# Performance work log

Hardware: AMD Instinct MI355X
Metric: run time of the kernel (lower is better)

Reference implementation:

```python
import jax, jax.numpy as jnp
import numpy as np

B, S, E, H = 2, 2048, 1024, 16
HD = E // H


def setup_inputs() -> dict:
    key = jax.random.key(0)
    ks = jax.random.split(key, 5)
    scale = 0.02
    return {
        "x": jax.random.normal(ks[0], (B, S, E), dtype=jnp.float32),
        "qkv_w": jax.random.normal(ks[1], (3 * E, E), dtype=jnp.float32) * scale,
        "qkv_b": jax.random.normal(ks[2], (3 * E,), dtype=jnp.float32) * scale,
        "out_w": jax.random.normal(ks[3], (E, E), dtype=jnp.float32) * scale,
        "out_b": jax.random.normal(ks[4], (E,), dtype=jnp.float32) * scale,
    }


def reference(x, qkv_w, qkv_b, out_w, out_b):
    b, s, e = x.shape
    scale = 1.0 / jnp.sqrt(jnp.float32(HD))
    # fused QKV projection: torch Linear is x @ W.T + b
    qkv = x @ qkv_w.T + qkv_b                       # [b, s, 3e]
    qkv = qkv.reshape(b, s, 3, H, HD)
    qkv = jnp.transpose(qkv, (2, 0, 3, 1, 4))       # [3, b, h, s, hd]
    q, k, v = qkv[0], qkv[1], qkv[2]
    scores = jnp.einsum('bhqd,bhkd->bhqk', q, k) * scale
    # causal mask (atmask=True): mask strictly upper triangle
    causal = jnp.triu(jnp.ones((s, s), dtype=bool), k=1)
    scores = jnp.where(causal, -jnp.inf, scores)
    attn = jax.nn.softmax(scores, axis=-1)          # dropout p=0.0 -> identity
    out = jnp.einsum('bhqk,bhkd->bhqd', attn, v)    # [b, h, s, hd]
    out = jnp.transpose(out, (0, 2, 1, 3)).reshape(b, s, e)
    return out @ out_w.T + out_b
```

## Files before the change

### kernel.cpp

```cpp
#include <hip/hip_runtime.h>
#include <cmath>

typedef __attribute__((ext_vector_type(8))) __bf16 bf16x8;
typedef __attribute__((ext_vector_type(8))) unsigned short ushort8v;
typedef __attribute__((ext_vector_type(4))) float f32x4;

__device__ inline unsigned short f2bf(float f) {
    unsigned int u = __float_as_uint(f);
    unsigned int r = (u + 0x7fffu + ((u >> 16) & 1u)) >> 16;
    return (unsigned short)r;
}

__device__ inline bf16x8 ld8(const unsigned short* p) {
    uint4 v = *(const uint4*)p;
    return __builtin_bit_cast(bf16x8, v);
}

__device__ inline f32x4 mfma16(bf16x8 a, bf16x8 b, f32x4 c) {
    return __builtin_amdgcn_mfma_f32_16x16x32_bf16(a, b, c, 0, 0, 0);
}

__device__ inline unsigned pk2t(float a, float b) {
    return __builtin_amdgcn_perm(__float_as_uint(b), __float_as_uint(a), 0x07060302u);
}

__device__ inline void store_out(float* C, size_t idx, float v) { C[idx] = v; }
__device__ inline void store_out(unsigned short* C, size_t idx, float v) { C[idx] = f2bf(v); }

__device__ inline void gl_lds16(const unsigned short* g, const unsigned short* l) {
    __builtin_amdgcn_global_load_lds(
        (const __attribute__((address_space(1))) void*)(unsigned long long)g,
        (__attribute__((address_space(3))) void*)(unsigned)(unsigned long long)l,
        16, 0, 0);
}

#define NX4  1048576
#define NW14 786432
#define NW24 262144
__global__ __launch_bounds__(256) void cvt3(const float* __restrict__ x,
                                            const float* __restrict__ w1,
                                            const float* __restrict__ w2,
                                            unsigned short* __restrict__ xb,
                                            unsigned short* __restrict__ w1b,
                                            unsigned short* __restrict__ w2b) {
    int i = blockIdx.x * 256 + threadIdx.x;
    const float* src;
    unsigned short* dst;
    int off;
    if (i < NX4)              { src = x;  dst = xb;  off = i; }
    else if (i < NX4 + NW14)  { src = w1; dst = w1b; off = i - NX4; }
    else                      { src = w2; dst = w2b; off = i - NX4 - NW14; }
    float4 v = ((const float4*)src)[off];
    ushort4 o;
    o.x = f2bf(v.x); o.y = f2bf(v.y); o.z = f2bf(v.z); o.w = f2bf(v.w);
    ((ushort4*)dst)[off] = o;
}

template <typename OutT>
__global__ __launch_bounds__(256) void gemm_bt(const unsigned short* __restrict__ A,
                                               const unsigned short* __restrict__ B,
                                               const float* __restrict__ bias,
                                               OutT* __restrict__ C,
                                               int M, int N, int K) {
    __shared__ __align__(16) unsigned short As[128 * 32];
    __shared__ __align__(16) unsigned short Bs[128 * 32];
    const int m0 = blockIdx.y * 128;
    const int n0 = blockIdx.x * 128;
    const int t = threadIdx.x;
    const int wave = t >> 6, lane = t & 63;
    const int l16 = lane & 15, quad = lane >> 4;
    const int wm = (wave >> 1) * 64, wn = (wave & 1) * 64;

    f32x4 acc[4][4] = {};

    const int c0 = t, c1 = 256 + t;
    const int r0 = c0 >> 2, kc0 = (c0 & 3) * 8;
    const int r1 = c1 >> 2, kc1 = (c1 & 3) * 8;

    for (int k0 = 0; k0 < K; k0 += 32) {
        __syncthreads();
        gl_lds16(A + (size_t)(m0 + r0) * K + k0 + kc0, As + c0 * 8);
        gl_lds16(B + (size_t)(n0 + r0) * K + k0 + kc0, Bs + c0 * 8);
        gl_lds16(A + (size_t)(m0 + r1) * K + k0 + kc1, As + c1 * 8);
        gl_lds16(B + (size_t)(n0 + r1) * K + k0 + kc1, Bs + c1 * 8);
        __syncthreads();

        bf16x8 af[4], bfr[4];
        #pragma unroll
        for (int i = 0; i < 4; ++i)
            af[i] = ld8(As + (wm + i * 16 + l16) * 32 + quad * 8);
        #pragma unroll
        for (int j = 0; j < 4; ++j)
            bfr[j] = ld8(Bs + (wn + j * 16 + l16) * 32 + quad * 8);
        #pragma unroll
        for (int i = 0; i < 4; ++i)
            #pragma unroll
            for (int j = 0; j < 4; ++j)
                acc[i][j] = mfma16(af[i], bfr[j], acc[i][j]);
    }

    #pragma unroll
    for (int i = 0; i < 4; ++i) {
        #pragma unroll
        for (int j = 0; j < 4; ++j) {
            int col = n0 + wn + j * 16 + l16;
            float bv = bias[col];
            #pragma unroll
            for (int r = 0; r < 4; ++r) {
                int row = m0 + wm + i * 16 + quad * 4 + r;
                store_out(C, (size_t)row * N + col, acc[i][j][r] + bv);
            }
        }
    }
}

__global__ __launch_bounds__(256) void gemm_qkv(const unsigned short* __restrict__ A,
                                                const unsigned short* __restrict__ B,
                                                const float* __restrict__ bias,
                                                unsigned short* __restrict__ qp,
                                                unsigned short* __restrict__ kvp,
                                                int M, int N, int K) {
    __shared__ __align__(16) unsigned short Ep[16384];
    unsigned short* As = Ep;
    unsigned short* Bs = Ep + 4096;
    const int m0 = blockIdx.y * 128;
    const int n0 = blockIdx.x * 128;
    const int t = threadIdx.x;
    const int wave = t >> 6, lane = t & 63;
    const int l16 = lane & 15, quad = lane >> 4;
    const int wm = (wave >> 1) * 64, wn = (wave & 1) * 64;

    f32x4 acc[4][4] = {};

    const int c0 = t, c1 = 256 + t;
    const int r0 = c0 >> 2, kc0 = (c0 & 3) * 8;
    const int r1 = c1 >> 2, kc1 = (c1 & 3) * 8;

    for (int k0 = 0; k0 < K; k0 += 32) {
        __syncthreads();
        gl_lds16(A + (size_t)(m0 + r0) * K + k0 + kc0, As + c0 * 8);
        gl_lds16(B + (size_t)(n0 + r0) * K + k0 + kc0, Bs + c0 * 8);
        gl_lds16(A + (size_t)(m0 + r1) * K + k0 + kc1, As + c1 * 8);
        gl_lds16(B + (size_t)(n0 + r1) * K + k0 + kc1, Bs + c1 * 8);
        __syncthreads();

        bf16x8 af[4], bfr[4];
        #pragma unroll
        for (int i = 0; i < 4; ++i)
            af[i] = ld8(As + (wm + i * 16 + l16) * 32 + quad * 8);
        #pragma unroll
        for (int j = 0; j < 4; ++j)
            bfr[j] = ld8(Bs + (wn + j * 16 + l16) * 32 + quad * 8);
        #pragma unroll
        for (int i = 0; i < 4; ++i)
            #pragma unroll
            for (int j = 0; j < 4; ++j)
                acc[i][j] = mfma16(af[i], bfr[j], acc[i][j]);
    }

    __syncthreads();
    const int b = m0 >> 11;

    if (n0 < 1024) {
        #pragma unroll
        for (int j = 0; j < 4; ++j) {
            int cl = wn + j * 16 + l16;
            float bv = bias[n0 + cl];
            int hrel = cl >> 6, d = cl & 63;
            int half = d >> 5, qd = d & 31;
            int obase = hrel * 8192 + half * 512 + (qd >> 3) * 128 + (qd & 7) + quad * 32;
            #pragma unroll
            for (int i = 0; i < 4; ++i) {
                int ob = obase + ((wm + i * 16) >> 4) * 1024;
                #pragma unroll
                for (int r = 0; r < 4; ++r)
                    Ep[ob + r * 8] = f2bf((acc[i][j][r] + bv) * 0.125f);
            }
        }
        __syncthreads();
        const int h0 = n0 >> 6, qt0 = (m0 & 2047) >> 4;
        #pragma unroll
        for (int k = 0; k < 8; ++k) {
            int u = t + 256 * k;
            int cq = u >> 7, within = u & 127;
            int bh = b * 16 + h0 + (cq >> 3);
            int qt = qt0 + (cq & 7);
            *(uint4*)(qp + (size_t)(bh * 128 + qt) * 1024 + within * 8) =
                *(const uint4*)(Ep + u * 8);
        }
    } else if (n0 < 2048) {
        const int f2 = (quad & 1) * 2, krow = quad >> 1;
        #pragma unroll
        for (int j = 0; j < 4; ++j) {
            int cl = wn + j * 16 + l16;
            float bv = bias[n0 + cl];
            int hrel = cl >> 6, d = cl & 63;
            int fbit0 = d >> 5, qd = d & 31;
            int obase = hrel * 8192 + (f2 | fbit0) * 512 + (qd >> 3) * 128 +
                        krow * 32 + (qd & 7);
            #pragma unroll
            for (int i = 0; i < 4; ++i) {
                int ob = obase + ((wm + i * 16) >> 5) * 2048 + (i & 1) * 64;
                #pragma unroll
                for (int r = 0; r < 4; ++r)
                    Ep[ob + r * 8] = f2bf(acc[i][j][r] + bv);
            }
        }
        __syncthreads();
        const int h0 = (n0 - 1024) >> 6, tile0 = (m0 & 2047) >> 5;
        #pragma unroll
        for (int k = 0; k < 8; ++k) {
            int u = t + 256 * k;
            int ck = u >> 8, within = u & 255;
            int bh = b * 16 + h0 + (ck >> 2);
            int tile = tile0 + (ck & 3);
            *(uint4*)(kvp + (size_t)(bh * 64 + tile) * 4096 + within * 8) =
                *(const uint4*)(Ep + u * 8);
        }
    } else {
        const int krow = quad >> 1, e4 = (quad & 1) * 4;
        #pragma unroll
        for (int j = 0; j < 4; ++j) {
            int cl = wn + j * 16 + l16;
            float bv = bias[n0 + cl];
            int hrel = cl >> 6, d = cl & 63;
            int tn = d >> 4, l16v = d & 15;
            int obase = hrel * 8192 + tn * 512 + (krow * 16 + l16v) * 8 + e4;
            #pragma unroll
            for (int i = 0; i < 4; ++i) {
                int ob = obase + ((wm + i * 16) >> 5) * 2048 + (i & 1) * 256;
                unsigned short tmp[4];
                #pragma unroll
                for (int r = 0; r < 4; ++r) tmp[r] = f2bf(acc[i][j][r] + bv);
                *(unsigned long long*)(Ep + ob) = *(const unsigned long long*)tmp;
            }
        }
        __syncthreads();
        const int h0 = (n0 - 2048) >> 6, tile0 = (m0 & 2047) >> 5;
        #pragma unroll
        for (int k = 0; k < 8; ++k) {
            int u = t + 256 * k;
            int ck = u >> 8, within = u & 255;
            int bh = b * 16 + h0 + (ck >> 2);
            int tile = tile0 + (ck & 3);
            *(uint4*)(kvp + (size_t)(bh * 64 + tile) * 4096 + 2048 + within * 8) =
                *(const uint4*)(Ep + u * 8);
        }
    }
}

__global__ __launch_bounds__(256, 3) void attn_kernel(const unsigned short* __restrict__ qp,
                                                      const unsigned short* __restrict__ kvp,
                                                      unsigned short* __restrict__ out) {
    const int S = 2048, E = 1024;
    const int wavei = threadIdx.x >> 6;
    const int lane = threadIdx.x & 63;
    const int l16 = lane & 15, quad = lane >> 4;
    const int bh = blockIdx.x & 31;
    const int P = 63 - (int)(blockIdx.x >> 5);
    const int b = bh >> 4, h = bh & 15;
    const int loff = lane * 8;

    const unsigned short* qbase = qp + ((size_t)(bh * 128 + 2 * P) * 2) * 512;
    bf16x8 bqA0 = ld8(qbase + loff);
    bf16x8 bqA1 = ld8(qbase + 512 + loff);
    bf16x8 bqB0 = ld8(qbase + 1024 + loff);
    bf16x8 bqB1 = ld8(qbase + 1536 + loff);

    ushort8v ov;
    #pragma unroll
    for (int j = 0; j < 8; ++j) ov[j] = 0x3F80;
    const bf16x8 ones = __builtin_bit_cast(bf16x8, ov);

    f32x4 OA[4] = {}, OB[4] = {};
    f32x4 LA = {}, LB = {};
    const int qA = 32 * P + l16, qB = qA + 16;
    const int nchunks = (P + 2) >> 1;
    const unsigned short* tbase = kvp + (size_t)bh * 64 * 4096;

    for (int c = wavei; c < nchunks; c += 4) {
        const unsigned short* tb = tbase + (size_t)c * 8192;
        bf16x8 f[16];
        #pragma unroll
        for (int i = 0; i < 16; ++i) f[i] = ld8(tb + i * 512 + loff);

        const bool lastc = (c == nchunks - 1);
        const int ks = c * 64;
        const bool skip1 = lastc && ((P & 1) == 0);

        #pragma unroll
        for (int tile = 0; tile < 2; ++tile) {
            if (tile == 1 && skip1) break;
            const bf16x8* g = f + tile * 8;
            const int kst = ks + tile * 32;

            f32x4 sA0 = {}, sA1 = {}, sB0 = {}, sB1 = {};
            sA0 = mfma16(g[0], bqA0, sA0);
            sA0 = mfma16(g[1], bqA1, sA0);
            sA1 = mfma16(g[2], bqA0, sA1);
            sA1 = mfma16(g[3], bqA1, sA1);
            sB0 = mfma16(g[0], bqB0, sB0);
            sB0 = mfma16(g[1], bqB1, sB0);
            sB1 = mfma16(g[2], bqB0, sB1);
            sB1 = mfma16(g[3], bqB1, sB1);

            float pA0[4], pA1[4], pB0[4], pB1[4];
            if (lastc) {
                #pragma unroll
                for (int r = 0; r < 4; ++r) {
                    int kk = kst + quad * 8 + r;
                    pA0[r] = (kk > qA)     ? 0.f : __expf(sA0[r]);
                    pA1[r] = (kk + 4 > qA) ? 0.f : __expf(sA1[r]);
                    pB0[r] = (kk > qB)     ? 0.f : __expf(sB0[r]);
                    pB1[r] = (kk + 4 > qB) ? 0.f : __expf(sB1[r]);
                }
            } else {
                #pragma unroll
                for (int r = 0; r < 4; ++r) {
                    pA0[r] = __expf(sA0[r]);
                    pA1[r] = __expf(sA1[r]);
                    pB0[r] = __expf(sB0[r]);
                    pB1[r] = __expf(sB1[r]);
                }
            }
            uint4 pwA, pwB;
            pwA.x = pk2t(pA0[0], pA0[1]);
            pwA.y = pk2t(pA0[2], pA0[3]);
            pwA.z = pk2t(pA1[0], pA1[1]);
            pwA.w = pk2t(pA1[2], pA1[3]);
            pwB.x = pk2t(pB0[0], pB0[1]);
            pwB.y = pk2t(pB0[2], pB0[3]);
            pwB.z = pk2t(pB1[0], pB1[1]);
            pwB.w = pk2t(pB1[2], pB1[3]);
            bf16x8 bpA = __builtin_bit_cast(bf16x8, pwA);
            bf16x8 bpB = __builtin_bit_cast(bf16x8, pwB);

            OA[0] = mfma16(g[4], bpA, OA[0]);
            OA[1] = mfma16(g[5], bpA, OA[1]);
            OA[2] = mfma16(g[6], bpA, OA[2]);
            OA[3] = mfma16(g[7], bpA, OA[3]);
            LA    = mfma16(ones, bpA, LA);
            OB[0] = mfma16(g[4], bpB, OB[0]);
            OB[1] = mfma16(g[5], bpB, OB[1]);
            OB[2] = mfma16(g[6], bpB, OB[2]);
            OB[3] = mfma16(g[7], bpB, OB[3]);
            LB    = mfma16(ones, bpB, LB);
        }
    }

    __shared__ float Ob[4][32][66];
    __shared__ float Lb[4][32];
    #pragma unroll
    for (int tn = 0; tn < 4; ++tn)
        #pragma unroll
        for (int r = 0; r < 4; ++r) {
            Ob[wavei][l16][tn * 16 + quad * 4 + r]      = OA[tn][r];
            Ob[wavei][16 + l16][tn * 16 + quad * 4 + r] = OB[tn][r];
        }
    if (quad == 0) {
        Lb[wavei][l16]      = LA[0];
        Lb[wavei][16 + l16] = LB[0];
    }
    __syncthreads();

    const int t = threadIdx.x;
    const int qi = t >> 3, hd0 = (t & 7) * 8;
    float ls = Lb[0][qi] + Lb[1][qi] + Lb[2][qi] + Lb[3][qi];
    const float invl = 1.0f / ls;
    unsigned short o[8];
    #pragma unroll
    for (int k = 0; k < 8; ++k) {
        float a = Ob[0][qi][hd0 + k] + Ob[1][qi][hd0 + k] +
                  Ob[2][qi][hd0 + k] + Ob[3][qi][hd0 + k];
        o[k] = f2bf(a * invl);
    }
    *(uint4*)(out + (size_t)(b * S + 32 * P + qi) * E + h * 64 + hd0) = *(uint4*)o;
}

extern "C" void kernel_launch(void* const* d_in, const int* in_sizes, int n_in,
                              void* d_out, int out_size, void* d_ws, size_t ws_size,
                              hipStream_t stream) {
    const float* x     = (const float*)d_in[0];
    const float* qkv_w = (const float*)d_in[1];
    const float* qkv_b = (const float*)d_in[2];
    const float* out_w = (const float*)d_in[3];
    const float* out_b = (const float*)d_in[4];
    float* out = (float*)d_out;

    const int B = 2, S = 2048, E = 1024;
    const int M = B * S;
    const int N1 = 3 * E;

    unsigned short* ws    = (unsigned short*)d_ws;
    unsigned short* xb    = ws;
    unsigned short* w1b   = xb   + (size_t)M * E;
    unsigned short* w2b   = w1b  + (size_t)N1 * E;
    unsigned short* qpb   = w2b  + (size_t)E * E;
    unsigned short* kvpb  = qpb  + (size_t)32 * 128 * 1024;
    unsigned short* attnb = kvpb + (size_t)32 * 64 * 4096;

    cvt3<<<dim3(8192), dim3(256), 0, stream>>>(x, qkv_w, out_w, xb, w1b, w2b);

    gemm_qkv<<<dim3(N1 / 128, M / 128), dim3(256), 0, stream>>>(
        xb, w1b, qkv_b, qpb, kvpb, M, N1, E);

    attn_kernel<<<dim3(2048), dim3(256), 0, stream>>>(qpb, kvpb, attnb);

    gemm_bt<float><<<dim3(E / 128, M / 128), dim3(256), 0, stream>>>(
        attnb, w2b, out_b, out, M, E, E);
}
```

Baseline: 187.5 us.

## Deepen GEMM K-steps, shrink out-proj tile, use exp2 softmax, remap attention blocks

Both GEMMs now load two 32-wide K slices per barrier pair (K step 64), which halves the number of __syncthreads per K pass. The output projection switches to 64x128 tiles so it launches more blocks and fills more CUs. The log2(e) factor is folded into the Q scale, so the attention kernel can call the hardware exp2 directly instead of __expf. Attention blocks are also remapped across batch-heads, which may change cache locality. In exchange the kernels use more LDS and registers per block, which could lower occupancy.

```diff
diff --git a/kernel.cpp b/kernel.cpp
--- a/kernel.cpp
+++ b/kernel.cpp
@@ -23,9 +23,6 @@
 __device__ inline unsigned pk2t(float a, float b) {
     return __builtin_amdgcn_perm(__float_as_uint(b), __float_as_uint(a), 0x07060302u);
 }
-
-__device__ inline void store_out(float* C, size_t idx, float v) { C[idx] = v; }
-__device__ inline void store_out(unsigned short* C, size_t idx, float v) { C[idx] = f2bf(v); }
 
 __device__ inline void gl_lds16(const unsigned short* g, const unsigned short* l) {
     __builtin_amdgcn_global_load_lds(
@@ -56,51 +53,67 @@
     ((ushort4*)dst)[off] = o;
 }
 
-template <typename OutT>
-__global__ __launch_bounds__(256) void gemm_bt(const unsigned short* __restrict__ A,
-                                               const unsigned short* __restrict__ B,
-                                               const float* __restrict__ bias,
-                                               OutT* __restrict__ C,
-                                               int M, int N, int K) {
-    __shared__ __align__(16) unsigned short As[128 * 32];
-    __shared__ __align__(16) unsigned short Bs[128 * 32];
-    const int m0 = blockIdx.y * 128;
+__global__ __launch_bounds__(256) void gemm_out(const unsigned short* __restrict__ A,
+                                                const unsigned short* __restrict__ B,
+                                                const float* __restrict__ bias,
+                                                float* __restrict__ C,
+                                                int M, int N, int K) {
+    __shared__ __align__(16) unsigned short As0[64 * 32];
+    __shared__ __align__(16) unsigned short Bs0[128 * 32];
+    __shared__ __align__(16) unsigned short As1[64 * 32];
+    __shared__ __align__(16) unsigned short Bs1[128 * 32];
+    const int m0 = blockIdx.y * 64;
     const int n0 = blockIdx.x * 128;
     const int t = threadIdx.x;
     const int wave = t >> 6, lane = t & 63;
     const int l16 = lane & 15, quad = lane >> 4;
-    const int wm = (wave >> 1) * 64, wn = (wave & 1) * 64;
-
-    f32x4 acc[4][4] = {};
-
-    const int c0 = t, c1 = 256 + t;
-    const int r0 = c0 >> 2, kc0 = (c0 & 3) * 8;
-    const int r1 = c1 >> 2, kc1 = (c1 & 3) * 8;
-
-    for (int k0 = 0; k0 < K; k0 += 32) {
-        __syncthreads();
-        gl_lds16(A + (size_t)(m0 + r0) * K + k0 + kc0, As + c0 * 8);
-        gl_lds16(B + (size_t)(n0 + r0) * K + k0 + kc0, Bs + c0 * 8);
-        gl_lds16(A + (size_t)(m0 + r1) * K + k0 + kc1, As + c1 * 8);
-        gl_lds16(B + (size_t)(n0 + r1) * K + k0 + kc1, Bs + c1 * 8);
-        __syncthreads();
-
-        bf16x8 af[4], bfr[4];
-        #pragma unroll
-        for (int i = 0; i < 4; ++i)
-            af[i] = ld8(As + (wm + i * 16 + l16) * 32 + quad * 8);
+    const int wm = (wave >> 1) * 32, wn = (wave & 1) * 64;
+
+    f32x4 acc[2][4] = {};
+
+    const int ra = t >> 2, ka = (t & 3) * 8;
+    const int b1 = 256 + t;
+    const int rb0 = t >> 2, kb0 = (t & 3) * 8;
+    const int rb1 = b1 >> 2, kb1 = (b1 & 3) * 8;
+
+    for (int k0 = 0; k0 < K; k0 += 64) {
+        __syncthreads();
+        gl_lds16(A + (size_t)(m0 + ra) * K + k0 + ka,        As0 + t * 8);
+        gl_lds16(B + (size_t)(n0 + rb0) * K + k0 + kb0,      Bs0 + t * 8);
+        gl_lds16(B + (size_t)(n0 + rb1) * K + k0 + kb1,      Bs0 + b1 * 8);
+        gl_lds16(A + (size_t)(m0 + ra) * K + k0 + 32 + ka,   As1 + t * 8);
+        gl_lds16(B + (size_t)(n0 + rb0) * K + k0 + 32 + kb0, Bs1 + t * 8);
+        gl_lds16(B + (size_t)(n0 + rb1) * K + k0 + 32 + kb1, Bs1 + b1 * 8);
+        __syncthreads();
+
+        bf16x8 af[2], bfr[4];
+        #pragma unroll
+        for (int i = 0; i < 2; ++i)
+            af[i] = ld8(As0 + (wm + i * 16 + l16) * 32 + quad * 8);
         #pragma unroll
         for (int j = 0; j < 4; ++j)
-            bfr[j] = ld8(Bs + (wn + j * 16 + l16) * 32 + quad * 8);
-        #pragma unroll
-        for (int i = 0; i < 4; ++i)
+            bfr[j] = ld8(Bs0 + (wn + j * 16 + l16) * 32 + quad * 8);
+        #pragma unroll
+        for (int i = 0; i < 2; ++i)
             #pragma unroll
             for (int j = 0; j < 4; ++j)
                 acc[i][j] = mfma16(af[i], bfr[j], acc[i][j]);
+
+        #pragma unroll
+        for (int i = 0; i < 2; ++i)
+            af[i] = ld8(As1 + (wm + i * 16 + l16) * 32 + quad * 8);
+        #pragma unroll
+        for (int j = 0; j < 4; ++j)
+            bfr[j] = ld8(Bs1 + (wn + j * 16 + l16) * 32 + quad * 8);
+        #pragma unroll
+        for (int i = 0; i < 2; ++i)
+            #pragma unroll
+            for (int j = 0; j < 4; ++j)
+                acc[i][j] = mfma16(af[i], bfr[j], acc[i][j]);
     }
 
     #pragma unroll
-    for (int i = 0; i < 4; ++i) {
+    for (int i = 0; i < 2; ++i) {
         #pragma unroll
         for (int j = 0; j < 4; ++j) {
             int col = n0 + wn + j * 16 + l16;
@@ -108,7 +121,7 @@
             #pragma unroll
             for (int r = 0; r < 4; ++r) {
                 int row = m0 + wm + i * 16 + quad * 4 + r;
-                store_out(C, (size_t)row * N + col, acc[i][j][r] + bv);
+                C[(size_t)row * N + col] = acc[i][j][r] + bv;
             }
         }
     }
@@ -121,8 +134,10 @@
                                                 unsigned short* __restrict__ kvp,
                                                 int M, int N, int K) {
     __shared__ __align__(16) unsigned short Ep[16384];
-    unsigned short* As = Ep;
-    unsigned short* Bs = Ep + 4096;
+    unsigned short* As0 = Ep;
+    unsigned short* Bs0 = Ep + 4096;
+    unsigned short* As1 = Ep + 8192;
+    unsigned short* Bs1 = Ep + 12288;
     const int m0 = blockIdx.y * 128;
     const int n0 = blockIdx.x * 128;
     const int t = threadIdx.x;
@@ -136,21 +151,37 @@
     const int r0 = c0 >> 2, kc0 = (c0 & 3) * 8;
     const int r1 = c1 >> 2, kc1 = (c1 & 3) * 8;
 
-    for (int k0 = 0; k0 < K; k0 += 32) {
-        __syncthreads();
-        gl_lds16(A + (size_t)(m0 + r0) * K + k0 + kc0, As + c0 * 8);
-        gl_lds16(B + (size_t)(n0 + r0) * K + k0 + kc0, Bs + c0 * 8);
-        gl_lds16(A + (size_t)(m0 + r1) * K + k0 + kc1, As + c1 * 8);
-        gl_lds16(B + (size_t)(n0 + r1) * K + k0 + kc1, Bs + c1 * 8);
+    for (int k0 = 0; k0 < K; k0 += 64) {
+        __syncthreads();
+        gl_lds16(A + (size_t)(m0 + r0) * K + k0 + kc0,      As0 + c0 * 8);
+        gl_lds16(B + (size_t)(n0 + r0) * K + k0 + kc0,      Bs0 + c0 * 8);
+        gl_lds16(A + (size_t)(m0 + r1) * K + k0 + kc1,      As0 + c1 * 8);
+        gl_lds16(B + (size_t)(n0 + r1) * K + k0 + kc1,      Bs0 + c1 * 8);
+        gl_lds16(A + (size_t)(m0 + r0) * K + k0 + 32 + kc0, As1 + c0 * 8);
+        gl_lds16(B + (size_t)(n0 + r0) * K + k0 + 32 + kc0, Bs1 + c0 * 8);
+        gl_lds16(A + (size_t)(m0 + r1) * K + k0 + 32 + kc1, As1 + c1 * 8);
+        gl_lds16(B + (size_t)(n0 + r1) * K + k0 + 32 + kc1, Bs1 + c1 * 8);
         __syncthreads();
 
         bf16x8 af[4], bfr[4];
         #pragma unroll
         for (int i = 0; i < 4; ++i)
-            af[i] = ld8(As + (wm + i * 16 + l16) * 32 + quad * 8);
+            af[i] = ld8(As0 + (wm + i * 16 + l16) * 32 + quad * 8);
         #pragma unroll
         for (int j = 0; j < 4; ++j)
-            bfr[j] = ld8(Bs + (wn + j * 16 + l16) * 32 + quad * 8);
+            bfr[j] = ld8(Bs0 + (wn + j * 16 + l16) * 32 + quad * 8);
+        #pragma unroll
+        for (int i = 0; i < 4; ++i)
+            #pragma unroll
+            for (int j = 0; j < 4; ++j)
+                acc[i][j] = mfma16(af[i], bfr[j], acc[i][j]);
+
+        #pragma unroll
+        for (int i = 0; i < 4; ++i)
+            af[i] = ld8(As1 + (wm + i * 16 + l16) * 32 + quad * 8);
+        #pragma unroll
+        for (int j = 0; j < 4; ++j)
+            bfr[j] = ld8(Bs1 + (wn + j * 16 + l16) * 32 + quad * 8);
         #pragma unroll
         for (int i = 0; i < 4; ++i)
             #pragma unroll
@@ -174,7 +205,7 @@
                 int ob = obase + ((wm + i * 16) >> 4) * 1024;
                 #pragma unroll
                 for (int r = 0; r < 4; ++r)
-                    Ep[ob + r * 8] = f2bf((acc[i][j][r] + bv) * 0.125f);
+                    Ep[ob + r * 8] = f2bf((acc[i][j][r] + bv) * 0.180336880f);
             }
         }
         __syncthreads();
@@ -256,8 +287,9 @@
     const int wavei = threadIdx.x >> 6;
     const int lane = threadIdx.x & 63;
     const int l16 = lane & 15, quad = lane >> 4;
-    const int bh = blockIdx.x & 31;
-    const int P = 63 - (int)(blockIdx.x >> 5);
+    const int bidx = blockIdx.x;
+    const int bh = (bidx & 7) * 4 + ((bidx >> 3) & 3);
+    const int P = 63 - (bidx >> 5);
     const int b = bh >> 4, h = bh & 15;
     const int loff = lane * 8;
 
@@ -309,18 +341,18 @@
                 #pragma unroll
                 for (int r = 0; r < 4; ++r) {
                     int kk = kst + quad * 8 + r;
-                    pA0[r] = (kk > qA)     ? 0.f : __expf(sA0[r]);
-                    pA1[r] = (kk + 4 > qA) ? 0.f : __expf(sA1[r]);
-                    pB0[r] = (kk > qB)     ? 0.f : __expf(sB0[r]);
-                    pB1[r] = (kk + 4 > qB) ? 0.f : __expf(sB1[r]);
+                    pA0[r] = (kk > qA)     ? 0.f : __builtin_amdgcn_exp2f(sA0[r]);
+                    pA1[r] = (kk + 4 > qA) ? 0.f : __builtin_amdgcn_exp2f(sA1[r]);
+                    pB0[r] = (kk > qB)     ? 0.f : __builtin_amdgcn_exp2f(sB0[r]);
+                    pB1[r] = (kk + 4 > qB) ? 0.f : __builtin_amdgcn_exp2f(sB1[r]);
                 }
             } else {
                 #pragma unroll
                 for (int r = 0; r < 4; ++r) {
-                    pA0[r] = __expf(sA0[r]);
-                    pA1[r] = __expf(sA1[r]);
-                    pB0[r] = __expf(sB0[r]);
-                    pB1[r] = __expf(sB1[r]);
+                    pA0[r] = __builtin_amdgcn_exp2f(sA0[r]);
+                    pA1[r] = __builtin_amdgcn_exp2f(sA1[r]);
+                    pB0[r] = __builtin_amdgcn_exp2f(sB0[r]);
+                    pB1[r] = __builtin_amdgcn_exp2f(sB1[r]);
                 }
             }
             uint4 pwA, pwB;
@@ -406,6 +438,6 @@
 
     attn_kernel<<<dim3(2048), dim3(256), 0, stream>>>(qpb, kvpb, attnb);
 
-    gemm_bt<float><<<dim3(E / 128, M / 128), dim3(256), 0, stream>>>(
+    gemm_out<<<dim3(E / 128, M / 64), dim3(256), 0, stream>>>(
         attnb, w2b, out_b, out, M, E, E);
 }
```

Result: faster. 172.4 us (-8.1%).
